# Optimization experiments

Hardware: AMD Instinct MI355X
Metric: run time of the kernel (lower is better)

Reference implementation:

```python
import jax, jax.numpy as jnp
import numpy as np

NPOINT, RADIUS, NSAMPLE = 1024, 0.2, 32
BN_EPS = 1e-5


def farthest_point_sample(xyz, npoint):
    # xyz: (B,N,3) -> (B,npoint) int32. Deterministic start at index 0
    # (torch version uses a random start; math is otherwise identical).
    B, N, _ = xyz.shape

    def step(carry, _):
        dist, farthest = carry
        centroid = jnp.take_along_axis(xyz, farthest[:, None, None], axis=1)  # (B,1,3)
        d = jnp.sum((xyz - centroid) ** 2, axis=-1)                            # (B,N)
        dist = jnp.minimum(dist, d)
        return (dist, jnp.argmax(dist, axis=-1).astype(jnp.int32)), farthest

    init = (jnp.full((B, N), 1e10, xyz.dtype), jnp.zeros((B,), jnp.int32))
    _, idxs = jax.lax.scan(step, init, None, length=npoint)
    return idxs.T  # (B, npoint)


def query_ball_point(radius, nsample, xyz, new_xyz):
    # xyz: (B,N,3), new_xyz: (B,S,3) -> (B,S,nsample) int32
    N = xyz.shape[1]
    sqrdists = jnp.sum((new_xyz[:, :, None, :] - xyz[:, None, :, :]) ** 2, axis=-1)  # (B,S,N)
    gi = jnp.where(sqrdists > radius ** 2, N, jnp.arange(N, dtype=jnp.int32))
    gi = jnp.sort(gi, axis=-1)[:, :, :nsample]
    first = gi[:, :, :1]
    return jnp.where(gi == N, first, gi)


def index_points_group(points, idx):
    # points: (B,N,C), idx: (B,S,K) -> (B,S,K,C)
    B, S, K = idx.shape
    flat = jnp.take_along_axis(points, idx.reshape(B, S * K)[..., None], axis=1)
    return flat.reshape(B, S, K, points.shape[-1])


def setup_inputs() -> dict:
    key = jax.random.key(0)
    ks = jax.random.split(key, 10)
    B, N, C = 16, 4096, 64
    mlp, cin = [64, 64, 128], 3 + C
    inp = {
        "xyz": jax.random.uniform(ks[0], (B, N, 3), jnp.float32),
        "points": jax.random.normal(ks[1], (B, N, C), jnp.float32),
    }
    last = cin
    for i, out in enumerate(mlp):
        inp[f"w{i}"] = jax.random.normal(ks[2 + i], (out, last), jnp.float32) * 0.05
        inp[f"b{i}"] = jnp.zeros((out,), jnp.float32)
        inp[f"g{i}"] = jnp.ones((out,), jnp.float32)
        inp[f"be{i}"] = jnp.zeros((out,), jnp.float32)
        last = out
    return inp


def _forward(xyz, points, params):
    fps_idx = farthest_point_sample(xyz, NPOINT)
    new_xyz = jnp.take_along_axis(xyz, fps_idx[..., None], axis=1)          # (B,S,3)
    idx = query_ball_point(RADIUS, NSAMPLE, xyz, new_xyz)                   # (B,S,K)
    grouped_xyz = index_points_group(xyz, idx)                              # (B,S,K,3)
    grouped_xyz_norm = (grouped_xyz - new_xyz[:, :, None, :]) / RADIUS
    gp = jnp.concatenate([grouped_xyz_norm, index_points_group(points, idx)], axis=-1)
    for (w, b, g, be) in params:
        h = jnp.einsum('bskc,oc->bsko', gp, w) + b                          # 1x1 conv
        mu = jnp.mean(h, axis=(0, 1, 2))
        var = jnp.var(h, axis=(0, 1, 2))                                    # biased, as BN training
        gp = jax.nn.relu((h - mu) * jax.lax.rsqrt(var + BN_EPS) * g + be)
    new_points = jnp.max(gp, axis=2)                                        # (B,S,C_out)
    return new_xyz, new_points


def reference(xyz, points, w0, b0, g0, be0, w1, b1, g1, be1, w2, b2, g2, be2):
    params = [(w0, b0, g0, be0), (w1, b1, g1, be1), (w2, b2, g2, be2)]
    return _forward(xyz, points, params)
```

## Files before the change

kernel.cpp:

```cpp
#include <hip/hip_runtime.h>
#include <stdint.h>

#define NB      16
#define NPTS    4096
#define CPTS    64
#define NPOINT  1024
#define NSAMPLE 32
#define NROWS   (NB*NPOINT*NSAMPLE)

__device__ __forceinline__ unsigned short f2bf(float f){
  uint32_t u = __float_as_uint(f);
  uint32_t r = u + 0x7fffu + ((u>>16)&1u);
  return (unsigned short)(r>>16);
}
__device__ __forceinline__ float bf2f(unsigned short u){ return __uint_as_float(((uint32_t)u)<<16); }
__device__ __forceinline__ float lo16(uint32_t d){ return __uint_as_float(d<<16); }
__device__ __forceinline__ float hi16(uint32_t d){ return __uint_as_float(d & 0xffff0000u); }
__device__ __forceinline__ uint32_t pack2(float a, float b){ return ((uint32_t)f2bf(b)<<16) | (uint32_t)f2bf(a); }

#define FMAX_DPP(m, CTRL) { \
  float _o = __uint_as_float((uint32_t)__builtin_amdgcn_update_dpp(0, (int)__float_as_uint(m), CTRL, 0xF, 0xF, true)); \
  m = fmaxf(m, _o); }

typedef __attribute__((ext_vector_type(8))) short bf16x8;
typedef __attribute__((ext_vector_type(4))) float f32x4;

__global__ __launch_bounds__(256) void fps_kernel(const float* __restrict__ xyz,
                                                  float* __restrict__ newxyz_f,
                                                  float* __restrict__ out){
  __shared__ float s_x[NPTS], s_y[NPTS], s_z[NPTS];
  __shared__ unsigned long long s_k[2][4];
  const int b = blockIdx.x, t = threadIdx.x;
  const float* Xb = xyz + (size_t)b*NPTS*3;
  float px[16], py[16], pz[16], dd[16];
  #pragma unroll
  for (int i=0;i<16;++i){
    int n = t*16+i;
    float x = Xb[n*3+0], y = Xb[n*3+1], z = Xb[n*3+2];
    px[i]=x; py[i]=y; pz[i]=z; dd[i]=1e10f;
    s_x[n]=x; s_y[n]=y; s_z[n]=z;
  }
  if (t==0){
    size_t o=(size_t)b*NPOINT*3;
    newxyz_f[o]=px[0]; newxyz_f[o+1]=py[0]; newxyz_f[o+2]=pz[0];
    out[o]=px[0]; out[o+1]=py[0]; out[o+2]=pz[0];
  }
  __syncthreads();
  float cx=s_x[0], cy=s_y[0], cz=s_z[0];
  const int lane = t&63, wid = t>>6;
  for (int s=1;s<NPOINT;++s){
    float bv=-1.0f; int bi=0;
    #pragma unroll
    for (int i=0;i<16;++i){
      float dx=__fsub_rn(px[i],cx), dy=__fsub_rn(py[i],cy), dz=__fsub_rn(pz[i],cz);
      float d=__fadd_rn(__fadd_rn(__fmul_rn(dx,dx),__fmul_rn(dy,dy)),__fmul_rn(dz,dz));
      float nd=fminf(dd[i],d); dd[i]=nd;
      if (nd>bv){ bv=nd; bi=t*16+i; }
    }
    float m = bv;
    FMAX_DPP(m,0x111)
    FMAX_DPP(m,0x112)
    FMAX_DPP(m,0x114)
    FMAX_DPP(m,0x118)
    FMAX_DPP(m,0x142)
    FMAX_DPP(m,0x143)
    float wm = __uint_as_float((uint32_t)__builtin_amdgcn_readlane((int)__float_as_uint(m), 63));
    unsigned long long mask = __ballot(bv==wm);
    int l = (int)__ffsll((unsigned long long)mask) - 1;
    int widx = __builtin_amdgcn_readlane(bi, l);
    const int buf = s&1;
    if (lane==0)
      s_k[buf][wid] = ((unsigned long long)__float_as_uint(wm)<<32) | (uint32_t)(~widx);
    __syncthreads();
    unsigned long long k0=s_k[buf][0], k1=s_k[buf][1], k2=s_k[buf][2], k3=s_k[buf][3];
    unsigned long long ka=(k0>k1)?k0:k1, kb=(k2>k3)?k2:k3;
    unsigned long long kf=(ka>kb)?ka:kb;
    int fi = (int)(~(uint32_t)(kf & 0xffffffffu));
    cx=s_x[fi]; cy=s_y[fi]; cz=s_z[fi];
    if (t==0){
      size_t o2=((size_t)b*NPOINT+s)*3;
      newxyz_f[o2]=cx; newxyz_f[o2+1]=cy; newxyz_f[o2+2]=cz;
      out[o2]=cx; out[o2+1]=cy; out[o2+2]=cz;
    }
  }
}

__global__ __launch_bounds__(256) void ballq_kernel(const float* __restrict__ xyz,
                                                    const float* __restrict__ newxyz_f,
                                                    int* __restrict__ ballidx){
  __shared__ float s_p[NPTS*3];
  __shared__ int s_list[4][NSAMPLE];
  const int b  = blockIdx.x >> 8;
  const int sg = blockIdx.x & 255;
  const int t = threadIdx.x;
  const float* Xb = xyz + (size_t)b*NPTS*3;
  {
    const float4* X4 = (const float4*)Xb;
    float4* S4 = (float4*)s_p;
    #pragma unroll
    for (int i=0;i<12;++i) S4[t + i*256] = X4[t + i*256];
  }
  __syncthreads();
  const int lane = t&63, wid = t>>6;
  const int s = sg*4 + wid;
  size_t co = ((size_t)b*NPOINT+s)*3;
  const float cx=newxyz_f[co], cy=newxyz_f[co+1], cz=newxyz_f[co+2];
  const float R2 = 0.04f;
  int count = 0;
  for (int j0=0; j0<NPTS && count<NSAMPLE; j0+=64){
    int j=j0+lane;
    float dx=__fsub_rn(cx,s_p[3*j]), dy=__fsub_rn(cy,s_p[3*j+1]), dz=__fsub_rn(cz,s_p[3*j+2]);
    float sq=__fadd_rn(__fadd_rn(__fmul_rn(dx,dx),__fmul_rn(dy,dy)),__fmul_rn(dz,dz));
    bool in = !(sq > R2);
    unsigned long long m = __ballot(in);
    int before = __popcll(m & ((1ull<<lane)-1ull));
    int pos = count + before;
    if (in && pos < NSAMPLE) s_list[wid][pos] = j;
    count += __popcll(m);
  }
  int c = count < NSAMPLE ? count : NSAMPLE;
  int first = s_list[wid][0];
  if (lane >= c && lane < NSAMPLE) s_list[wid][lane] = first;
  if (lane < NSAMPLE) ballidx[((size_t)b*NPOINT+s)*NSAMPLE + lane] = s_list[wid][lane];
}

#define L1_STRIDE 71
__global__ __launch_bounds__(256,3) void layer1_kernel(const float* __restrict__ xyz,
    const float* __restrict__ points, const int* __restrict__ ballidx,
    const float* __restrict__ newxyz_f, const float* __restrict__ w0,
    const float* __restrict__ b0, unsigned short* __restrict__ h){
  __shared__ float s_w[67*32];
  __shared__ float s_b[32];
  __shared__ float s_x[128*L1_STRIDE];
  __shared__ int   s_j[128];
  const int t = threadIdx.x;
  const int tile = blockIdx.x >> 1;
  const int half = blockIdx.x & 1;
  const int tileBase = tile*128;
  for (int i=t;i<67*32;i+=256){
    int c=i>>5, oL=i&31;
    int srcc = (c<64) ? (c+3) : (c-64);
    s_w[i] = w0[(half*32+oL)*67 + srcc];
  }
  if (t<32) s_b[t]=b0[half*32+t];
  if (t<128) s_j[t]=ballidx[tileBase+t];
  __syncthreads();
  #pragma unroll
  for (int it=0; it<8; ++it){
    int r = it*16 + (t>>4);
    int row = tileBase + r;
    int bb = row >> 15;
    int j  = s_j[r];
    float4 pv = *(const float4*)(points + ((size_t)bb*NPTS + (size_t)j)*CPTS + (t&15)*4);
    float* xr = s_x + r*L1_STRIDE + (t&15)*4;
    xr[0]=pv.x; xr[1]=pv.y; xr[2]=pv.z; xr[3]=pv.w;
  }
  if (t<128){
    int row = tileBase + t;
    int bs  = row >> 5;
    int bb  = bs >> 10;
    int j   = s_j[t];
    const float* xr = xyz + ((size_t)bb*NPTS + (size_t)j)*3;
    const float* cp = newxyz_f + (size_t)bs*3;
    float* xd = s_x + t*L1_STRIDE + 64;
    xd[0]=(xr[0]-cp[0])/0.2f; xd[1]=(xr[1]-cp[1])/0.2f; xd[2]=(xr[2]-cp[2])/0.2f;
  }
  __syncthreads();
  const int r    = t & 127;
  const int osub = (t>>7)*16;
  const float* xp = s_x + r*L1_STRIDE;
  float acc[16];
  #pragma unroll
  for (int o=0;o<16;++o) acc[o]=0.0f;
  for (int c=0;c<67;++c){
    float xv = xp[c];
    const float4* wr=(const float4*)(s_w + c*32 + osub);
    #pragma unroll
    for (int q=0;q<4;++q){ float4 w=wr[q];
      acc[4*q+0]=fmaf(xv,w.x,acc[4*q+0]); acc[4*q+1]=fmaf(xv,w.y,acc[4*q+1]);
      acc[4*q+2]=fmaf(xv,w.z,acc[4*q+2]); acc[4*q+3]=fmaf(xv,w.w,acc[4*q+3]); }
  }
  uint4* od=(uint4*)(h + (size_t)(tileBase+r)*64 + half*32 + osub);
  #pragma unroll
  for (int q=0;q<2;++q){
    uint4 v;
    v.x=pack2(acc[8*q+0]+s_b[osub+8*q+0], acc[8*q+1]+s_b[osub+8*q+1]);
    v.y=pack2(acc[8*q+2]+s_b[osub+8*q+2], acc[8*q+3]+s_b[osub+8*q+3]);
    v.z=pack2(acc[8*q+4]+s_b[osub+8*q+4], acc[8*q+5]+s_b[osub+8*q+5]);
    v.w=pack2(acc[8*q+6]+s_b[osub+8*q+6], acc[8*q+7]+s_b[osub+8*q+7]);
    od[q]=v;
  }
}

__global__ __launch_bounds__(256) void stats64_kernel(const unsigned short* __restrict__ h,
                                                      float* __restrict__ st){
  __shared__ float s_red[4][64][8], s_red2[4][64][8];
  const int t=threadIdx.x, lane=t&63, wid=t>>6;
  const int gw = blockIdx.x*4+wid;
  const int rsub = lane>>3;
  float sm[8], sq[8];
  #pragma unroll
  for (int j=0;j<8;++j){ sm[j]=0.f; sq[j]=0.f; }
  for (int it=0; it<32; ++it){
    size_t row = (size_t)gw*256 + it*8 + rsub;
    const uint4* p = (const uint4*)(h + row*64) + (lane&7);
    uint4 v = *p;
    uint32_t ds4[4]={v.x,v.y,v.z,v.w};
    #pragma unroll
    for (int dj=0;dj<4;++dj){
      float a=lo16(ds4[dj]), b2=hi16(ds4[dj]);
      sm[2*dj]+=a;   sq[2*dj]  =fmaf(a,a,sq[2*dj]);
      sm[2*dj+1]+=b2; sq[2*dj+1]=fmaf(b2,b2,sq[2*dj+1]);
    }
  }
  #pragma unroll
  for (int j=0;j<8;++j){ s_red[wid][lane][j]=sm[j]; s_red2[wid][lane][j]=sq[j]; }
  __syncthreads();
  if (t<64){
    float ts=0.f,tq=0.f;
    #pragma unroll
    for (int w=0;w<4;++w)
      #pragma unroll
      for (int m=0;m<8;++m){ int l=(t>>3)+8*m; ts+=s_red[w][l][t&7]; tq+=s_red2[w][l][t&7]; }
    atomicAdd(&st[t*2], ts); atomicAdd(&st[t*2+1], tq);
  }
}

__global__ __launch_bounds__(256,3) void layer2_kernel(unsigned short* __restrict__ h,
    const float* __restrict__ st, const float* __restrict__ g,
    const float* __restrict__ be, const float* __restrict__ w1,
    const float* __restrict__ b1){
  __shared__ float s_w[64*64];
  __shared__ float s_x[128*65];
  __shared__ float s_b[64], s_scale[64], s_shift[64];
  const int t=threadIdx.x;
  const int tileBase = blockIdx.x*128;
  for (int i=t;i<64*64;i+=256){ int c=i>>6, o=i&63; s_w[i]=w1[o*64+c]; }
  if (t<64){
    s_b[t]=b1[t];
    float mu=st[t*2]*(1.0f/NROWS);
    float var=st[t*2+1]*(1.0f/NROWS)-mu*mu;
    float inv=1.0f/sqrtf(var+1e-5f);
    s_scale[t]=inv*g[t]; s_shift[t]=be[t]-mu*inv*g[t];
  }
  __syncthreads();
  #pragma unroll
  for (int it=0; it<4; ++it){
    int idx = it*256 + t;
    int r = idx>>3, seg = idx&7;
    uint4 v = *((const uint4*)(h + (size_t)(tileBase+r)*64) + seg);
    float* xd = s_x + r*65 + seg*8;
    uint32_t ds4[4]={v.x,v.y,v.z,v.w};
    #pragma unroll
    for (int dj=0;dj<4;++dj){
      int c = seg*8 + dj*2;
      xd[dj*2+0]=fmaxf(fmaf(lo16(ds4[dj]),s_scale[c],  s_shift[c]),  0.0f);
      xd[dj*2+1]=fmaxf(fmaf(hi16(ds4[dj]),s_scale[c+1],s_shift[c+1]),0.0f);
    }
  }
  __syncthreads();
  const int r    = t & 127;
  const int osub = (t>>7)*32;
  const float* xp = s_x + r*65;
  float acc[32];
  #pragma unroll
  for (int o=0;o<32;++o) acc[o]=0.0f;
  for (int c=0;c<64;++c){
    float xv = xp[c];
    const float4* wr=(const float4*)(s_w + c*64 + osub);
    #pragma unroll
    for (int q=0;q<8;++q){ float4 w=wr[q];
      acc[4*q+0]=fmaf(xv,w.x,acc[4*q+0]); acc[4*q+1]=fmaf(xv,w.y,acc[4*q+1]);
      acc[4*q+2]=fmaf(xv,w.z,acc[4*q+2]); acc[4*q+3]=fmaf(xv,w.w,acc[4*q+3]); }
  }
  uint4* od=(uint4*)(h + (size_t)(tileBase+r)*64 + osub);
  #pragma unroll
  for (int q=0;q<4;++q){
    uint4 v;
    v.x=pack2(acc[8*q+0]+s_b[osub+8*q+0], acc[8*q+1]+s_b[osub+8*q+1]);
    v.y=pack2(acc[8*q+2]+s_b[osub+8*q+2], acc[8*q+3]+s_b[osub+8*q+3]);
    v.z=pack2(acc[8*q+4]+s_b[osub+8*q+4], acc[8*q+5]+s_b[osub+8*q+5]);
    v.w=pack2(acc[8*q+6]+s_b[osub+8*q+6], acc[8*q+7]+s_b[osub+8*q+7]);
    od[q]=v;
  }
}

__global__ __launch_bounds__(256,2) void layer3mm_kernel(const unsigned short* __restrict__ h,
    const float* __restrict__ st, const float* __restrict__ g,
    const float* __restrict__ be, const float* __restrict__ w2,
    const float* __restrict__ b2, float* __restrict__ mm, float* __restrict__ part){
  __shared__ __align__(16) unsigned short s_wB[8192];
  __shared__ unsigned short s_t[4][32*136+8];
  __shared__ float s_scale[64], s_shift[64], s_b2[128];
  const int t=threadIdx.x, lane=t&63, wid=t>>6;
  const int quad=lane>>4, n15=lane&15;
  for (int i=t;i<8192;i+=256){
    int j=i&7, nn=(i>>3)&15, qq=(i>>7)&3, nt=(i>>9)&7, kt=(i>>12)&1;
    s_wB[i] = f2bf(w2[(nt*16+nn)*64 + (kt*32+qq*8+j)]);
  }
  if (t<64){
    float mu=st[t*2]*(1.0f/NROWS);
    float var=st[t*2+1]*(1.0f/NROWS)-mu*mu;
    float inv=1.0f/sqrtf(var+1e-5f);
    s_scale[t]=inv*g[t]; s_shift[t]=be[t]-mu*inv*g[t];
  }
  if (t<128) s_b2[t]=b2[t];
  __syncthreads();
  float sc[16], sh[16];
  #pragma unroll
  for (int j=0;j<8;++j){
    sc[j]   = s_scale[quad*8+j];    sh[j]   = s_shift[quad*8+j];
    sc[8+j] = s_scale[32+quad*8+j]; sh[8+j] = s_shift[32+quad*8+j];
  }
  unsigned short* tile = s_t[wid];
  #pragma unroll 1
  for (int i2=0;i2<2;++i2){
    const int sg = blockIdx.x*8 + wid*2 + i2;
    const int rowBase = sg*32;
    bf16x8 A[2][2];
    #pragma unroll
    for (int rt=0;rt<2;++rt){
      const unsigned short* hp = h + (size_t)(rowBase + rt*16 + n15)*64 + quad*8;
      #pragma unroll
      for (int kt=0;kt<2;++kt){
        uint4 v = *(const uint4*)(hp + kt*32);
        uint32_t d4[4]={v.x,v.y,v.z,v.w};
        #pragma unroll
        for (int dj=0;dj<4;++dj){
          float xa=fmaxf(fmaf(lo16(d4[dj]),sc[kt*8+dj*2],  sh[kt*8+dj*2]),  0.0f);
          float xb=fmaxf(fmaf(hi16(d4[dj]),sc[kt*8+dj*2+1],sh[kt*8+dj*2+1]),0.0f);
          A[rt][kt][dj*2]   = (short)f2bf(xa);
          A[rt][kt][dj*2+1] = (short)f2bf(xb);
        }
      }
    }
    #pragma unroll
    for (int nt=0;nt<8;++nt){
      bf16x8 B0 = *(const bf16x8*)&s_wB[((nt*4+quad)*16+n15)*8];
      bf16x8 B1 = *(const bf16x8*)&s_wB[(((8+nt)*4+quad)*16+n15)*8];
      f32x4 a0={0.f,0.f,0.f,0.f}, a1={0.f,0.f,0.f,0.f};
      a0 = __builtin_amdgcn_mfma_f32_16x16x32_bf16(A[0][0],B0,a0,0,0,0);
      a0 = __builtin_amdgcn_mfma_f32_16x16x32_bf16(A[0][1],B1,a0,0,0,0);
      a1 = __builtin_amdgcn_mfma_f32_16x16x32_bf16(A[1][0],B0,a1,0,0,0);
      a1 = __builtin_amdgcn_mfma_f32_16x16x32_bf16(A[1][1],B1,a1,0,0,0);
      float bias = s_b2[nt*16+n15];
      #pragma unroll
      for (int r=0;r<4;++r){
        tile[(quad*4+r)*136    + nt*16+n15] = f2bf(a0[r]+bias);
        tile[(16+quad*4+r)*136 + nt*16+n15] = f2bf(a1[r]+bias);
      }
    }
    float mxA=-3e38f,mnA=3e38f,sA=0.f,qA=0.f;
    float mxB=-3e38f,mnB=3e38f,sB=0.f,qB=0.f;
    #pragma unroll
    for (int r=0;r<32;++r){
      float va=bf2f(tile[r*136+lane]);
      float vb=bf2f(tile[r*136+lane+64]);
      mxA=fmaxf(mxA,va); mnA=fminf(mnA,va); sA+=va; qA=fmaf(va,va,qA);
      mxB=fmaxf(mxB,vb); mnB=fminf(mnB,vb); sB+=vb; qB=fmaf(vb,vb,qB);
    }
    float* mp = mm + (size_t)sg*256;
    mp[lane]=mxA;     mp[lane+64]=mxB;
    mp[128+lane]=mnA; mp[192+lane]=mnB;
    part[(size_t)sg*256+lane]=sA;      part[(size_t)sg*256+64+lane]=sB;
    part[(size_t)sg*256+128+lane]=qA;  part[(size_t)sg*256+192+lane]=qB;
  }
}

__global__ __launch_bounds__(256) void reduce_kernel(const float* __restrict__ part,
                                                     float* __restrict__ st2){
  const int t=threadIdx.x;
  const int base = blockIdx.x*64;
  float acc=0.f;
  for (int r=0;r<64;++r) acc += part[(size_t)(base+r)*256 + t];
  if (t<128) atomicAdd(&st2[t*2], acc);
  else       atomicAdd(&st2[(t-128)*2+1], acc);
}

__global__ __launch_bounds__(256) void final_kernel(const float* __restrict__ mm,
    const float* __restrict__ st, const float* __restrict__ g,
    const float* __restrict__ be, float* __restrict__ out){
  __shared__ float s_scale[128], s_shift[128];
  const int t=threadIdx.x;
  if (t<128){
    float mu=st[t*2]*(1.0f/NROWS);
    float var=st[t*2+1]*(1.0f/NROWS)-mu*mu;
    float inv=1.0f/sqrtf(var+1e-5f);
    s_scale[t]=inv*g[t]; s_shift[t]=be[t]-mu*inv*g[t];
  }
  __syncthreads();
  const int idx = blockIdx.x*256+t;
  const int ch = idx & 127, bs = idx >> 7;
  float sc=s_scale[ch];
  float v = (sc>=0.f)? mm[(size_t)bs*256+ch] : mm[(size_t)bs*256+128+ch];
  out[(size_t)NB*NPOINT*3 + idx] = fmaxf(fmaf(v,sc,s_shift[ch]),0.0f);
}

extern "C" void kernel_launch(void* const* d_in, const int* in_sizes, int n_in,
                              void* d_out, int out_size, void* d_ws, size_t ws_size,
                              hipStream_t stream) {
  const float* xyz    = (const float*)d_in[0];
  const float* points = (const float*)d_in[1];
  const float* w0 = (const float*)d_in[2];
  const float* b0 = (const float*)d_in[3];
  const float* g0 = (const float*)d_in[4];
  const float* be0= (const float*)d_in[5];
  const float* w1 = (const float*)d_in[6];
  const float* b1 = (const float*)d_in[7];
  const float* g1 = (const float*)d_in[8];
  const float* be1= (const float*)d_in[9];
  const float* w2 = (const float*)d_in[10];
  const float* b2 = (const float*)d_in[11];
  const float* g2 = (const float*)d_in[12];
  const float* be2= (const float*)d_in[13];
  float* out = (float*)d_out;
  char* ws = (char*)d_ws;

  float* newxyz_f = (float*)(ws);
  int*   ballidx  = (int*)(ws + 196608);
  float* stats    = (float*)(ws + 2293760);
  float* mm       = (float*)(ws + 4194304);
  unsigned short* h = (unsigned short*)(ws + 20971520);
  float* part     = (float*)(ws + 88080384);

  hipMemsetAsync(stats, 0, 3072, stream);
  hipLaunchKernelGGL(fps_kernel,     dim3(NB),    dim3(256), 0, stream, xyz, newxyz_f, out);
  hipLaunchKernelGGL(ballq_kernel,   dim3(4096),  dim3(256), 0, stream, xyz, newxyz_f, ballidx);
  hipLaunchKernelGGL(layer1_kernel,  dim3(8192),  dim3(256), 0, stream,
                     xyz, points, ballidx, newxyz_f, w0, b0, h);
  hipLaunchKernelGGL(stats64_kernel, dim3(512),   dim3(256), 0, stream, h, stats + 0);
  hipLaunchKernelGGL(layer2_kernel,  dim3(4096),  dim3(256), 0, stream,
                     h, stats + 0, g0, be0, w1, b1);
  hipLaunchKernelGGL(stats64_kernel, dim3(512),   dim3(256), 0, stream, h, stats + 256);
  hipLaunchKernelGGL(layer3mm_kernel,dim3(2048),  dim3(256), 0, stream,
                     h, stats + 256, g1, be1, w2, b2, mm, part);
  hipLaunchKernelGGL(reduce_kernel,  dim3(256),   dim3(256), 0, stream, part, stats + 512);
  hipLaunchKernelGGL(final_kernel,   dim3(8192),  dim3(256), 0, stream,
                     mm, stats + 512, g2, be2, out);
}
```

Before: 1.075 ms.

## Use bf16 MFMA for layer 2 and fuse its BN statistics into the kernel

Replaces the scalar FP32 FMA layer-2 1x1 conv with bf16 MFMA 16x16x32 instructions, modelled on the existing layer-3 kernel. Per-32-row-group sums and sums of squares are computed in-kernel into a partials buffer and reduced by a small reduce kernel. This removes the separate stats64 pass that re-read h. The cost is that inputs to the layer-2 matmul are now rounded to bf16, which loses some precision.

Result: faster. 978.2 us (-9.0%).

```diff
diff --git a/kernel.cpp b/kernel.cpp
--- a/kernel.cpp
+++ b/kernel.cpp
@@ -226,63 +226,97 @@
   }
 }
 
-__global__ __launch_bounds__(256,3) void layer2_kernel(unsigned short* __restrict__ h,
+__global__ __launch_bounds__(256,2) void layer2mm_kernel(unsigned short* __restrict__ h,
     const float* __restrict__ st, const float* __restrict__ g,
     const float* __restrict__ be, const float* __restrict__ w1,
-    const float* __restrict__ b1){
-  __shared__ float s_w[64*64];
-  __shared__ float s_x[128*65];
-  __shared__ float s_b[64], s_scale[64], s_shift[64];
-  const int t=threadIdx.x;
-  const int tileBase = blockIdx.x*128;
-  for (int i=t;i<64*64;i+=256){ int c=i>>6, o=i&63; s_w[i]=w1[o*64+c]; }
+    const float* __restrict__ b1, float* __restrict__ part2){
+  __shared__ __align__(16) unsigned short s_wB[4096];
+  __shared__ __align__(16) unsigned short s_t[4][32*72+8];
+  __shared__ float s_scale[64], s_shift[64], s_b[64];
+  const int t=threadIdx.x, lane=t&63, wid=t>>6;
+  const int quad=lane>>4, n15=lane&15;
+  for (int i=t;i<4096;i+=256){
+    int j=i&7, nn=(i>>3)&15, qq=(i>>7)&3, nt=(i>>9)&3, kt=(i>>11)&1;
+    s_wB[i] = f2bf(w1[(nt*16+nn)*64 + (kt*32+qq*8+j)]);
+  }
   if (t<64){
-    s_b[t]=b1[t];
     float mu=st[t*2]*(1.0f/NROWS);
     float var=st[t*2+1]*(1.0f/NROWS)-mu*mu;
     float inv=1.0f/sqrtf(var+1e-5f);
     s_scale[t]=inv*g[t]; s_shift[t]=be[t]-mu*inv*g[t];
-  }
-  __syncthreads();
-  #pragma unroll
-  for (int it=0; it<4; ++it){
-    int idx = it*256 + t;
-    int r = idx>>3, seg = idx&7;
-    uint4 v = *((const uint4*)(h + (size_t)(tileBase+r)*64) + seg);
-    float* xd = s_x + r*65 + seg*8;
-    uint32_t ds4[4]={v.x,v.y,v.z,v.w};
-    #pragma unroll
-    for (int dj=0;dj<4;++dj){
-      int c = seg*8 + dj*2;
-      xd[dj*2+0]=fmaxf(fmaf(lo16(ds4[dj]),s_scale[c],  s_shift[c]),  0.0f);
-      xd[dj*2+1]=fmaxf(fmaf(hi16(ds4[dj]),s_scale[c+1],s_shift[c+1]),0.0f);
-    }
-  }
-  __syncthreads();
-  const int r    = t & 127;
-  const int osub = (t>>7)*32;
-  const float* xp = s_x + r*65;
-  float acc[32];
-  #pragma unroll
-  for (int o=0;o<32;++o) acc[o]=0.0f;
-  for (int c=0;c<64;++c){
-    float xv = xp[c];
-    const float4* wr=(const float4*)(s_w + c*64 + osub);
-    #pragma unroll
-    for (int q=0;q<8;++q){ float4 w=wr[q];
-      acc[4*q+0]=fmaf(xv,w.x,acc[4*q+0]); acc[4*q+1]=fmaf(xv,w.y,acc[4*q+1]);
-      acc[4*q+2]=fmaf(xv,w.z,acc[4*q+2]); acc[4*q+3]=fmaf(xv,w.w,acc[4*q+3]); }
-  }
-  uint4* od=(uint4*)(h + (size_t)(tileBase+r)*64 + osub);
-  #pragma unroll
-  for (int q=0;q<4;++q){
-    uint4 v;
-    v.x=pack2(acc[8*q+0]+s_b[osub+8*q+0], acc[8*q+1]+s_b[osub+8*q+1]);
-    v.y=pack2(acc[8*q+2]+s_b[osub+8*q+2], acc[8*q+3]+s_b[osub+8*q+3]);
-    v.z=pack2(acc[8*q+4]+s_b[osub+8*q+4], acc[8*q+5]+s_b[osub+8*q+5]);
-    v.w=pack2(acc[8*q+6]+s_b[osub+8*q+6], acc[8*q+7]+s_b[osub+8*q+7]);
-    od[q]=v;
-  }
+    s_b[t]=b1[t];
+  }
+  __syncthreads();
+  float sc[16], sh[16];
+  #pragma unroll
+  for (int j=0;j<8;++j){
+    sc[j]   = s_scale[quad*8+j];    sh[j]   = s_shift[quad*8+j];
+    sc[8+j] = s_scale[32+quad*8+j]; sh[8+j] = s_shift[32+quad*8+j];
+  }
+  unsigned short* tile = s_t[wid];
+  #pragma unroll 1
+  for (int i2=0;i2<2;++i2){
+    const int sg = blockIdx.x*8 + wid*2 + i2;
+    const int rowBase = sg*32;
+    bf16x8 A[2][2];
+    #pragma unroll
+    for (int rt=0;rt<2;++rt){
+      const unsigned short* hp = h + (size_t)(rowBase + rt*16 + n15)*64 + quad*8;
+      #pragma unroll
+      for (int kt=0;kt<2;++kt){
+        uint4 v = *(const uint4*)(hp + kt*32);
+        uint32_t d4[4]={v.x,v.y,v.z,v.w};
+        #pragma unroll
+        for (int dj=0;dj<4;++dj){
+          float xa=fmaxf(fmaf(lo16(d4[dj]),sc[kt*8+dj*2],  sh[kt*8+dj*2]),  0.0f);
+          float xb=fmaxf(fmaf(hi16(d4[dj]),sc[kt*8+dj*2+1],sh[kt*8+dj*2+1]),0.0f);
+          A[rt][kt][dj*2]   = (short)f2bf(xa);
+          A[rt][kt][dj*2+1] = (short)f2bf(xb);
+        }
+      }
+    }
+    #pragma unroll
+    for (int nt=0;nt<4;++nt){
+      bf16x8 B0 = *(const bf16x8*)&s_wB[(((0*4+nt)*4+quad)*16+n15)*8];
+      bf16x8 B1 = *(const bf16x8*)&s_wB[(((1*4+nt)*4+quad)*16+n15)*8];
+      f32x4 a0={0.f,0.f,0.f,0.f}, a1={0.f,0.f,0.f,0.f};
+      a0 = __builtin_amdgcn_mfma_f32_16x16x32_bf16(A[0][0],B0,a0,0,0,0);
+      a0 = __builtin_amdgcn_mfma_f32_16x16x32_bf16(A[0][1],B1,a0,0,0,0);
+      a1 = __builtin_amdgcn_mfma_f32_16x16x32_bf16(A[1][0],B0,a1,0,0,0);
+      a1 = __builtin_amdgcn_mfma_f32_16x16x32_bf16(A[1][1],B1,a1,0,0,0);
+      float bias = s_b[nt*16+n15];
+      #pragma unroll
+      for (int r=0;r<4;++r){
+        tile[(quad*4+r)*72    + nt*16+n15] = f2bf(a0[r]+bias);
+        tile[(16+quad*4+r)*72 + nt*16+n15] = f2bf(a1[r]+bias);
+      }
+    }
+    float sA=0.f,qA=0.f;
+    #pragma unroll
+    for (int r=0;r<32;++r){
+      float v=bf2f(tile[r*72+lane]);
+      sA+=v; qA=fmaf(v,v,qA);
+    }
+    part2[(size_t)sg*128+lane]    = sA;
+    part2[(size_t)sg*128+64+lane] = qA;
+    #pragma unroll
+    for (int tk=0;tk<4;++tk){
+      int task = tk*64 + lane;
+      int row = task>>3, q = task&7;
+      uint4 v = *(const uint4*)&tile[row*72 + q*8];
+      *(uint4*)(h + (size_t)(rowBase+row)*64 + q*8) = v;
+    }
+  }
+}
+
+__global__ __launch_bounds__(128) void reduce64_kernel(const float* __restrict__ part2,
+                                                       float* __restrict__ st){
+  const int t=threadIdx.x;
+  const int base = blockIdx.x*128;
+  float acc=0.f;
+  for (int r=0;r<128;++r) acc += part2[(size_t)(base+r)*128 + t];
+  if (t<64) atomicAdd(&st[t*2], acc);
+  else      atomicAdd(&st[(t-64)*2+1], acc);
 }
 
 __global__ __launch_bounds__(256,2) void layer3mm_kernel(const unsigned short* __restrict__ h,
@@ -429,9 +463,9 @@
   hipLaunchKernelGGL(layer1_kernel,  dim3(8192),  dim3(256), 0, stream,
                      xyz, points, ballidx, newxyz_f, w0, b0, h);
   hipLaunchKernelGGL(stats64_kernel, dim3(512),   dim3(256), 0, stream, h, stats + 0);
-  hipLaunchKernelGGL(layer2_kernel,  dim3(4096),  dim3(256), 0, stream,
-                     h, stats + 0, g0, be0, w1, b1);
-  hipLaunchKernelGGL(stats64_kernel, dim3(512),   dim3(256), 0, stream, h, stats + 256);
+  hipLaunchKernelGGL(layer2mm_kernel,dim3(2048),  dim3(256), 0, stream,
+                     h, stats + 0, g0, be0, w1, b1, part);
+  hipLaunchKernelGGL(reduce64_kernel,dim3(128),   dim3(128), 0, stream, part, stats + 256);
   hipLaunchKernelGGL(layer3mm_kernel,dim3(2048),  dim3(256), 0, stream,
                      h, stats + 256, g1, be1, w2, b2, mm, part);
   hipLaunchKernelGGL(reduce_kernel,  dim3(256),   dim3(256), 0, stream, part, stats + 512);
```
